# Optimization experiments

Measured on AMD Instinct MI355X. Metric: run time of the kernel, lower is better.

Reference implementation:

```python
import jax, jax.numpy as jnp
import numpy as np

TAU_S = 2.0  # fixed in the original module


def setup_inputs() -> dict:
    key = jax.random.key(0)
    T, N, C = 64, 512, 2048
    inputs = jax.random.normal(key, (T, N, C), dtype=jnp.float32)
    return {"inputs": inputs}


def reference(inputs):
    # syn_t = syn_{t-1} + (x_t - syn_{t-1}) / tau_s
    #       = syn_{t-1} * (1 - 1/tau) + x_t / tau, syn_{-1} = 0
    decay = jnp.asarray(1.0 - 1.0 / TAU_S, dtype=inputs.dtype)
    inv_tau = jnp.asarray(1.0 / TAU_S, dtype=inputs.dtype)

    def step(syn, x_t):
        syn = syn * decay + x_t * inv_tau
        return syn, syn

    syn0 = jnp.zeros(inputs.shape[1:], dtype=inputs.dtype)
    _, syns = jax.lax.scan(step, syn0, inputs)
    return syns  # (T, N, C)
```

## Files before the change

### kernel.cpp

```cpp
#include <hip/hip_runtime.h>


#define T_STEPS 64
#define NC (512 * 2048)
#define NC4 (NC / 4)

__global__ __launch_bounds__(256) void psp_scan_kernel(
    const float4* __restrict__ in, float4* __restrict__ out) {
    const int idx = blockIdx.x * blockDim.x + threadIdx.x;
    const float4* ip = in + idx;
    float4* op = out + idx;

    float sx = 0.f, sy = 0.f, sz = 0.f, sw = 0.f;
#pragma unroll 8
    for (int t = 0; t < T_STEPS; ++t) {
        const float4 x = ip[(size_t)t * NC4];
        sx = 0.5f * (sx + x.x);
        sy = 0.5f * (sy + x.y);
        sz = 0.5f * (sz + x.z);
        sw = 0.5f * (sw + x.w);
        op[(size_t)t * NC4] = make_float4(sx, sy, sz, sw);
    }
}

extern "C" void kernel_launch(void* const* d_in, const int* in_sizes, int n_in,
                              void* d_out, int out_size, void* d_ws, size_t ws_size,
                              hipStream_t stream) {
    const float4* in = (const float4*)d_in[0];
    float4* out = (float4*)d_out;
    psp_scan_kernel<<<NC4 / 256, 256, 0, stream>>>(in, out);
}
```

Before: 447.1 us.

## Double-buffer timestep loads in registers and use nontemporal stores

Restructures the time loop into batches of eight timesteps with two register buffers, so the loads for the next batch are issued before the current batch is computed and stored. This keeps more loads in flight per thread to hide memory latency. Output stores also become nontemporal to avoid polluting the cache with write-once data. More live registers are used, which could lower occupancy.

```diff
diff --git a/kernel.cpp b/kernel.cpp
--- a/kernel.cpp
+++ b/kernel.cpp
@@ -1,32 +1,66 @@
 #include <hip/hip_runtime.h>
 
 
+typedef float f4 __attribute__((ext_vector_type(4)));
+
 #define T_STEPS 64
-#define NC (512 * 2048)
-#define NC4 (NC / 4)
+#define NC4 (512 * 2048 / 4)
+#define BATCH 8
+
+__device__ __forceinline__ void load_batch(const f4* __restrict__ ip, int base,
+                                           f4 (&x)[BATCH]) {
+#pragma unroll
+    for (int j = 0; j < BATCH; ++j)
+        x[j] = ip[(size_t)(base + j) * (size_t)NC4];
+}
+
+__device__ __forceinline__ void compute_store(f4* __restrict__ op, int base,
+                                              f4 (&x)[BATCH], f4& acc) {
+#pragma unroll
+    for (int j = 0; j < BATCH; ++j) {
+        acc = 0.5f * (acc + x[j]);
+        __builtin_nontemporal_store(acc, &op[(size_t)(base + j) * (size_t)NC4]);
+    }
+}
 
 __global__ __launch_bounds__(256) void psp_scan_kernel(
-    const float4* __restrict__ in, float4* __restrict__ out) {
+    const f4* __restrict__ in, f4* __restrict__ out) {
     const int idx = blockIdx.x * blockDim.x + threadIdx.x;
-    const float4* ip = in + idx;
-    float4* op = out + idx;
+    const f4* ip = in + idx;
+    f4* op = out + idx;
 
-    float sx = 0.f, sy = 0.f, sz = 0.f, sw = 0.f;
-#pragma unroll 8
-    for (int t = 0; t < T_STEPS; ++t) {
-        const float4 x = ip[(size_t)t * NC4];
-        sx = 0.5f * (sx + x.x);
-        sy = 0.5f * (sy + x.y);
-        sz = 0.5f * (sz + x.z);
-        sw = 0.5f * (sw + x.w);
-        op[(size_t)t * NC4] = make_float4(sx, sy, sz, sw);
-    }
+    f4 A[BATCH], B[BATCH];
+    f4 acc = {0.f, 0.f, 0.f, 0.f};
+
+    load_batch(ip, 0 * BATCH, A);
+    load_batch(ip, 1 * BATCH, B);
+
+    compute_store(op, 0 * BATCH, A, acc);
+    load_batch(ip, 2 * BATCH, A);
+
+    compute_store(op, 1 * BATCH, B, acc);
+    load_batch(ip, 3 * BATCH, B);
+
+    compute_store(op, 2 * BATCH, A, acc);
+    load_batch(ip, 4 * BATCH, A);
+
+    compute_store(op, 3 * BATCH, B, acc);
+    load_batch(ip, 5 * BATCH, B);
+
+    compute_store(op, 4 * BATCH, A, acc);
+    load_batch(ip, 6 * BATCH, A);
+
+    compute_store(op, 5 * BATCH, B, acc);
+    load_batch(ip, 7 * BATCH, B);
+
+    compute_store(op, 6 * BATCH, A, acc);
+    compute_store(op, 7 * BATCH, B, acc);
 }
 
 extern "C" void kernel_launch(void* const* d_in, const int* in_sizes, int n_in,
                               void* d_out, int out_size, void* d_ws, size_t ws_size,
                               hipStream_t stream) {
-    const float4* in = (const float4*)d_in[0];
-    float4* out = (float4*)d_out;
+    const f4* in = (const f4*)d_in[0];
+    f4* out = (f4*)d_out;
     psp_scan_kernel<<<NC4 / 256, 256, 0, stream>>>(in, out);
 }
```

Measured after the change: 487.5 us. 9.0% more time.

## Split time scan into parallel chunks with shared-memory carry propagation

Applied to the files above, without the earlier changes.

Each block now handles 64 column vectors with four thread groups, each scanning a 16-step time chunk. All chunk loads are issued up front to raise memory-level parallelism. Chunk finals are exchanged through shared memory and a decayed carry is added before the stores. This gives four times more threads and removes the long serial load chain, at the cost of more registers and a block barrier.

```diff
diff --git a/kernel.cpp b/kernel.cpp
--- a/kernel.cpp
+++ b/kernel.cpp
@@ -1,32 +1,55 @@
 #include <hip/hip_runtime.h>
 
 
-#define T_STEPS 64
-#define NC (512 * 2048)
-#define NC4 (NC / 4)
+typedef float f4 __attribute__((ext_vector_type(4)));
+
+#define NC4 (512 * 2048 / 4)
+#define CHUNK 16
+#define NCHUNK 4
+#define COLS 64
 
 __global__ __launch_bounds__(256) void psp_scan_kernel(
-    const float4* __restrict__ in, float4* __restrict__ out) {
-    const int idx = blockIdx.x * blockDim.x + threadIdx.x;
-    const float4* ip = in + idx;
-    float4* op = out + idx;
+    const f4* __restrict__ in, f4* __restrict__ out) {
+    const int col   = threadIdx.x & (COLS - 1);
+    const int chunk = threadIdx.x >> 6;
+    const int colIdx = blockIdx.x * COLS + col;
 
-    float sx = 0.f, sy = 0.f, sz = 0.f, sw = 0.f;
-#pragma unroll 8
-    for (int t = 0; t < T_STEPS; ++t) {
-        const float4 x = ip[(size_t)t * NC4];
-        sx = 0.5f * (sx + x.x);
-        sy = 0.5f * (sy + x.y);
-        sz = 0.5f * (sz + x.z);
-        sw = 0.5f * (sw + x.w);
-        op[(size_t)t * NC4] = make_float4(sx, sy, sz, sw);
+    const f4* ip = in  + (size_t)(chunk * CHUNK) * NC4 + colIdx;
+    f4*       op = out + (size_t)(chunk * CHUNK) * NC4 + colIdx;
+
+    f4 v[CHUNK];
+#pragma unroll
+    for (int j = 0; j < CHUNK; ++j)
+        v[j] = ip[(size_t)j * NC4];
+
+    f4 acc = {0.f, 0.f, 0.f, 0.f};
+#pragma unroll
+    for (int j = 0; j < CHUNK; ++j) {
+        acc = 0.5f * (acc + v[j]);
+        v[j] = acc;
+    }
+
+    __shared__ f4 finals[NCHUNK][COLS];
+    finals[chunk][col] = acc;
+    __syncthreads();
+
+    f4 carry = {0.f, 0.f, 0.f, 0.f};
+    if (chunk >= 1) carry = finals[chunk - 1][col];
+    if (chunk >= 2) carry += finals[chunk - 2][col] * 0x1p-16f;
+    if (chunk >= 3) carry += finals[chunk - 3][col] * 0x1p-32f;
+
+    float d = 0.5f;
+#pragma unroll
+    for (int j = 0; j < CHUNK; ++j) {
+        op[(size_t)j * NC4] = v[j] + carry * d;
+        d *= 0.5f;
     }
 }
 
 extern "C" void kernel_launch(void* const* d_in, const int* in_sizes, int n_in,
                               void* d_out, int out_size, void* d_ws, size_t ws_size,
                               hipStream_t stream) {
-    const float4* in = (const float4*)d_in[0];
-    float4* out = (float4*)d_out;
-    psp_scan_kernel<<<NC4 / 256, 256, 0, stream>>>(in, out);
+    const f4* in = (const f4*)d_in[0];
+    f4* out = (f4*)d_out;
+    psp_scan_kernel<<<NC4 / COLS, 256, 0, stream>>>(in, out);
 }
```

Result: faster. 435.7 us (-2.5%).
